# Optimization experiments

Hardware: AMD Instinct MI355X
Metric: run time of the kernel (lower is better)

Reference implementation:

```python
import jax, jax.numpy as jnp
import numpy as np

D_MODEL, N_HEADS, D_LLM = 1024, 16, 4096
D_KEYS = D_MODEL // N_HEADS  # 64


def setup_inputs() -> dict:
    key = jax.random.key(0)
    ks = jax.random.split(key, 11)
    s = lambda fan_in: 1.0 / np.sqrt(fan_in)
    inp = {
        "target_embedding": jax.random.normal(ks[0], (4, 2048, D_MODEL), jnp.float32),
        "source_embedding": jax.random.normal(ks[1], (4, 1024, D_LLM), jnp.float32),
        "value_embedding": jax.random.normal(ks[2], (4, 1024, D_LLM), jnp.float32),
        "Wq": jax.random.uniform(ks[3], (D_MODEL, D_KEYS * N_HEADS), jnp.float32, -s(D_MODEL), s(D_MODEL)),
        "bq": jax.random.uniform(ks[4], (D_KEYS * N_HEADS,), jnp.float32, -s(D_MODEL), s(D_MODEL)),
        "Wk": jax.random.uniform(ks[5], (D_LLM, D_KEYS * N_HEADS), jnp.float32, -s(D_LLM), s(D_LLM)),
        "bk": jax.random.uniform(ks[6], (D_KEYS * N_HEADS,), jnp.float32, -s(D_LLM), s(D_LLM)),
        "Wv": jax.random.uniform(ks[7], (D_LLM, D_KEYS * N_HEADS), jnp.float32, -s(D_LLM), s(D_LLM)),
        "bv": jax.random.uniform(ks[8], (D_KEYS * N_HEADS,), jnp.float32, -s(D_LLM), s(D_LLM)),
        "Wo": jax.random.uniform(ks[9], (D_KEYS * N_HEADS, D_MODEL), jnp.float32, -s(D_KEYS * N_HEADS), s(D_KEYS * N_HEADS)),
        "bo": jax.random.uniform(ks[10], (D_MODEL,), jnp.float32, -s(D_KEYS * N_HEADS), s(D_KEYS * N_HEADS)),
    }
    return inp


def reference(target_embedding, source_embedding, value_embedding,
              Wq, bq, Wk, bk, Wv, bv, Wo, bo):
    B, L, _ = target_embedding.shape
    _, S, _ = source_embedding.shape
    H, E = N_HEADS, D_KEYS
    q = (target_embedding @ Wq + bq).reshape(B, L, H, E)
    k = (source_embedding @ Wk + bk).reshape(B, S, H, E)
    v = (value_embedding @ Wv + bv).reshape(B, S, H, E)
    scale = 1.0 / np.sqrt(E)
    scores = jnp.einsum('blhe,bshe->bhls', q, k)  # [B,H,L,S]
    A = jax.nn.softmax(scale * scores, axis=-1)   # dropout = identity (eval mode)
    out = jnp.einsum('bhls,bshe->blhe', A, v).reshape(B, L, H * E)
    return out @ Wo + bo
```

## Files before the change

kernel.cpp:

```cpp
#include <hip/hip_runtime.h>
#include <hip/hip_bf16.h>

using bf16 = __hip_bfloat16;
typedef __attribute__((ext_vector_type(8))) short short8;
typedef __attribute__((ext_vector_type(4))) float f32x4;

static constexpr int Bc = 4, Lc = 2048, Sc = 1024;
static constexpr int DModel = 1024;

__device__ __forceinline__ void gload16(const void* g, void* l) {
  __builtin_amdgcn_global_load_lds((const __attribute__((address_space(1))) void*)g,
                                   (__attribute__((address_space(3))) void*)l,
                                   16, 0, 0);
}

__global__ void cvt3(const float* __restrict__ a, bf16* __restrict__ ao, long na4,
                     const float* __restrict__ b, bf16* __restrict__ bo, long nb4,
                     const float* __restrict__ c, bf16* __restrict__ co, long nc4) {
  long total = na4 + nb4 + nc4;
  long stride = (long)gridDim.x * blockDim.x;
  for (long i = (long)blockIdx.x * blockDim.x + threadIdx.x; i < total; i += stride) {
    const float* src; bf16* dst; long j;
    if (i < na4)            { src = a; dst = ao; j = i; }
    else if (i < na4 + nb4) { src = b; dst = bo; j = i - na4; }
    else                    { src = c; dst = co; j = i - na4 - nb4; }
    float4 v = reinterpret_cast<const float4*>(src)[j];
    alignas(8) bf16 t[4] = {__float2bfloat16(v.x), __float2bfloat16(v.y),
                            __float2bfloat16(v.z), __float2bfloat16(v.w)};
    reinterpret_cast<ushort4*>(dst)[j] = *reinterpret_cast<const ushort4*>(t);
  }
}

__global__ __launch_bounds__(256) void transpose_cvt_w(const float* __restrict__ Wq, bf16* __restrict__ WqT,
                                                       const float* __restrict__ Wk, bf16* __restrict__ WkT,
                                                       const float* __restrict__ Wv, bf16* __restrict__ WvT,
                                                       const float* __restrict__ Wo, bf16* __restrict__ WoT) {
  __shared__ bf16 tile[32][33];
  int bid = blockIdx.x;
  const float* in; bf16* out; int R, l;
  if (bid < 1024)      { in = Wq; out = WqT; R = 1024; l = bid; }
  else if (bid < 5120) { in = Wk; out = WkT; R = 4096; l = bid - 1024; }
  else if (bid < 9216) { in = Wv; out = WvT; R = 4096; l = bid - 5120; }
  else                 { in = Wo; out = WoT; R = 1024; l = bid - 9216; }
  const int C = 1024;
  int bx = l & 31, by = l >> 5;
  int tx = threadIdx.x & 31, ty = threadIdx.x >> 5;
  int r0 = by * 32, c0 = bx * 32;
#pragma unroll
  for (int i = 0; i < 32; i += 8)
    tile[ty + i][tx] = __float2bfloat16(in[(long)(r0 + ty + i) * C + c0 + tx]);
  __syncthreads();
#pragma unroll
  for (int i = 0; i < 32; i += 8)
    out[(long)(c0 + ty + i) * R + r0 + tx] = tile[tx][ty + i];
}

__device__ __forceinline__ void gemm_core(const bf16* __restrict__ A, const bf16* __restrict__ Bt,
                                          const float* __restrict__ bias,
                                          bf16* __restrict__ Cb, float* __restrict__ Cf,
                                          bf16* __restrict__ Cvt,
                                          int N, int K, int bx, int by,
                                          bf16* As, bf16* Bs) {
  const int tid = threadIdx.x;
  const int lane = tid & 63, g = lane >> 4, lm = lane & 15;
  const int wid = tid >> 6, wr = wid >> 1, wc = wid & 1;
  const long brow = (long)by * 128, bcol = (long)bx * 128;

  const bf16* asrc[4];
  const bf16* bsrc[4];
  int dsto[4];
#pragma unroll
  for (int t = 0; t < 4; ++t) {
    int sl = tid + t * 256;
    int row = sl >> 3;
    int kg = (sl & 7) ^ (row & 7);
    asrc[t] = A + (brow + row) * (long)K + kg * 8;
    bsrc[t] = Bt + (bcol + row) * (long)K + kg * 8;
    dsto[t] = sl * 16;
  }

  f32x4 zero = {0.f, 0.f, 0.f, 0.f};
  f32x4 acc[4][4];
#pragma unroll
  for (int i = 0; i < 4; ++i)
#pragma unroll
    for (int j = 0; j < 4; ++j) acc[i][j] = zero;

  char* Asc = (char*)As;
  char* Bsc = (char*)Bs;

#pragma unroll
  for (int t = 0; t < 4; ++t) {
    gload16(asrc[t], Asc + dsto[t]);
    gload16(bsrc[t], Bsc + dsto[t]);
    asrc[t] += 64; bsrc[t] += 64;
  }
  __syncthreads();

  const int nt = K >> 6;
  for (int i = 0; i < nt; ++i) {
    const int cur = i & 1;
    if (i + 1 < nt) {
      const int nxt = cur ^ 1;
#pragma unroll
      for (int t = 0; t < 4; ++t) {
        gload16(asrc[t], Asc + nxt * 16384 + dsto[t]);
        gload16(bsrc[t], Bsc + nxt * 16384 + dsto[t]);
        asrc[t] += 64; bsrc[t] += 64;
      }
    }
    const char* Ab = Asc + cur * 16384;
    const char* Bb = Bsc + cur * 16384;
    __builtin_amdgcn_s_setprio(1);
#pragma unroll
    for (int ks = 0; ks < 2; ++ks) {
      short8 af[4], bfv[4];
#pragma unroll
      for (int mi = 0; mi < 4; ++mi) {
        int m = wr * 64 + mi * 16 + lm;
        af[mi] = *reinterpret_cast<const short8*>(
            Ab + ((m * 128 + ks * 64 + g * 16) ^ ((m & 7) << 4)));
      }
#pragma unroll
      for (int ni = 0; ni < 4; ++ni) {
        int n = wc * 64 + ni * 16 + lm;
        bfv[ni] = *reinterpret_cast<const short8*>(
            Bb + ((n * 128 + ks * 64 + g * 16) ^ ((n & 7) << 4)));
      }
#pragma unroll
      for (int mi = 0; mi < 4; ++mi)
#pragma unroll
        for (int ni = 0; ni < 4; ++ni)
          acc[mi][ni] = __builtin_amdgcn_mfma_f32_16x16x32_bf16(af[mi], bfv[ni], acc[mi][ni], 0, 0, 0);
    }
    __builtin_amdgcn_s_setprio(0);
    __syncthreads();
  }

#pragma unroll
  for (int ni = 0; ni < 4; ++ni) {
    long n = bcol + wc * 64 + ni * 16 + lm;
    float bv = bias ? bias[n] : 0.f;
#pragma unroll
    for (int mi = 0; mi < 4; ++mi) {
      long m0 = brow + wr * 64 + mi * 16 + g * 4;
      if (Cvt) {
        long b = m0 >> 10, s0 = m0 & 1023;
        alignas(8) bf16 t4[4];
#pragma unroll
        for (int r = 0; r < 4; ++r) t4[r] = __float2bfloat16(acc[mi][ni][r] + bv);
        *reinterpret_cast<ushort4*>(Cvt + ((b << 10) + n) * 1024 + s0) =
            *reinterpret_cast<const ushort4*>(t4);
      } else {
#pragma unroll
        for (int r = 0; r < 4; ++r) {
          float o = acc[mi][ni][r] + bv;
          if (Cb) Cb[(m0 + r) * N + n] = __float2bfloat16(o);
          else    Cf[(m0 + r) * N + n] = o;
        }
      }
    }
  }
}

__global__ __launch_bounds__(256) void gemm_bt(const bf16* __restrict__ A,
                                               const bf16* __restrict__ Bt,
                                               const float* __restrict__ bias,
                                               bf16* __restrict__ Cb,
                                               float* __restrict__ Cf,
                                               int N, int K) {
  __shared__ bf16 As[2 * 128 * 64];
  __shared__ bf16 Bs[2 * 128 * 64];
  gemm_core(A, Bt, bias, Cb, Cf, nullptr, N, K, blockIdx.x, blockIdx.y, As, Bs);
}

__global__ __launch_bounds__(256) void gemm_qkv(
    const bf16* __restrict__ Ak, const bf16* __restrict__ Bk, const float* __restrict__ bk_, bf16* __restrict__ Ck, int Kk, int nbk,
    const bf16* __restrict__ Av, const bf16* __restrict__ Bv_, const float* __restrict__ bv_, bf16* __restrict__ CvT, int Kv, int nbv,
    const bf16* __restrict__ Aq, const bf16* __restrict__ Bq_, const float* __restrict__ bq_, bf16* __restrict__ Cq, int Kq) {
  __shared__ bf16 As[2 * 128 * 64];
  __shared__ bf16 Bs[2 * 128 * 64];
  int bid = blockIdx.x;
  const bf16 *A, *Bt; const float* bias; bf16 *C = nullptr, *Cvt = nullptr; int K, l;
  if (bid < nbk)            { A = Ak; Bt = Bk;  bias = bk_; C = Ck;    K = Kk; l = bid; }
  else if (bid < nbk + nbv) { A = Av; Bt = Bv_; bias = bv_; Cvt = CvT; K = Kv; l = bid - nbk; }
  else                      { A = Aq; Bt = Bq_; bias = bq_; C = Cq;   K = Kq; l = bid - nbk - nbv; }
  gemm_core(A, Bt, bias, C, nullptr, Cvt, 1024, K, l & 7, l >> 3, As, Bs);
}

__global__ __launch_bounds__(256) void attn_fused(const bf16* __restrict__ q,
                                                  const bf16* __restrict__ k,
                                                  const bf16* __restrict__ vT,
                                                  bf16* __restrict__ o) {
  constexpr float C2 = 0.18033688011112042f;
  constexpr float THR = 6.0f;
  __shared__ bf16 Kl[2][64 * 64];
  __shared__ bf16 Vl[2][64 * 64];
  __shared__ bf16 Pl[4][16 * 64];
  const int tid = threadIdx.x;
  const int lane = tid & 63, g = lane >> 4, lm = lane & 15;
  const int wid = tid >> 6;
  const int b = blockIdx.y >> 4, h = blockIdx.y & 15;
  const int qbase = blockIdx.x * 64 + wid * 16;

  const bf16* qrow = q + (long)(b * Lc + qbase + lm) * DModel + h * 64;
  short8 qa0 = *reinterpret_cast<const short8*>(qrow + g * 8);
  short8 qa1 = *reinterpret_cast<const short8*>(qrow + 32 + g * 8);
#pragma unroll
  for (int j = 0; j < 8; ++j) {
    union { ushort u; bf16 h; } cv;
    cv.u = (ushort)qa0[j];
    bf16 s0 = __float2bfloat16(__bfloat162float(cv.h) * C2);
    qa0[j] = (short)*reinterpret_cast<ushort*>(&s0);
    cv.u = (ushort)qa1[j];
    bf16 s1 = __float2bfloat16(__bfloat162float(cv.h) * C2);
    qa1[j] = (short)*reinterpret_cast<ushort*>(&s1);
  }

  const bf16* kbase = k + (long)b * Sc * DModel + h * 64;
  const bf16* vbase = vT + ((long)b * DModel + h * 64) * Sc;

  const bf16* ksrc[2];
  const bf16* vsrc[2];
  int dsto[2];
#pragma unroll
  for (int t = 0; t < 2; ++t) {
    int sl = tid + t * 256;
    int row = sl >> 3;
    int cg = (sl & 7) ^ (row & 7);
    ksrc[t] = kbase + (long)row * DModel + cg * 8;
    vsrc[t] = vbase + (long)row * Sc + cg * 8;
    dsto[t] = sl * 16;
  }

  f32x4 zero = {0.f, 0.f, 0.f, 0.f};
  f32x4 accO[4];
#pragma unroll
  for (int i = 0; i < 4; ++i) accO[i] = zero;
  f32x4 accL = zero;
  float mst[4] = {-1e30f, -1e30f, -1e30f, -1e30f};

  short8 vones;
#pragma unroll
  for (int j = 0; j < 8; ++j) vones[j] = (short)0x3F80;

  char* Klc = (char*)Kl;
  char* Vlc = (char*)Vl;
  char* Plc = (char*)Pl + wid * (16 * 64 * 2);

#pragma unroll
  for (int t = 0; t < 2; ++t) {
    gload16(ksrc[t], Klc + dsto[t]);
    gload16(vsrc[t], Vlc + dsto[t]);
    ksrc[t] += 64 * DModel; vsrc[t] += 64;
  }
  __syncthreads();

  for (int j = 0; j < Sc / 64; ++j) {
    const int cur = j & 1;
    if (j + 1 < Sc / 64) {
      const int nxt = cur ^ 1;
#pragma unroll
      for (int t = 0; t < 2; ++t) {
        gload16(ksrc[t], Klc + nxt * 8192 + dsto[t]);
        gload16(vsrc[t], Vlc + nxt * 8192 + dsto[t]);
        ksrc[t] += 64 * DModel; vsrc[t] += 64;
      }
    }
    const char* Kb = Klc + cur * 8192;
    const char* Vb = Vlc + cur * 8192;

    f32x4 scv[4];
    __builtin_amdgcn_s_setprio(1);
#pragma unroll
    for (int st = 0; st < 4; ++st) {
      int s = st * 16 + lm;
      int sw = (s & 7) << 4;
      short8 kb0 = *reinterpret_cast<const short8*>(Kb + ((s * 128 + g * 16) ^ sw));
      short8 kb1 = *reinterpret_cast<const short8*>(Kb + ((s * 128 + 64 + g * 16) ^ sw));
      f32x4 z = zero;
      z = __builtin_amdgcn_mfma_f32_16x16x32_bf16(qa0, kb0, z, 0, 0, 0);
      z = __builtin_amdgcn_mfma_f32_16x16x32_bf16(qa1, kb1, z, 0, 0, 0);
      scv[st] = z;
    }
    __builtin_amdgcn_s_setprio(0);

    float pmax[4];
#pragma unroll
    for (int r = 0; r < 4; ++r)
      pmax[r] = fmaxf(fmaxf(scv[0][r], scv[1][r]), fmaxf(scv[2][r], scv[3][r]));
    int need = 0;
#pragma unroll
    for (int r = 0; r < 4; ++r) need |= (pmax[r] > mst[r] + THR) ? 1 : 0;
    if (__any(need)) {
#pragma unroll
      for (int r = 0; r < 4; ++r) {
        float mx = pmax[r];
        mx = fmaxf(mx, __shfl_xor(mx, 1));
        mx = fmaxf(mx, __shfl_xor(mx, 2));
        mx = fmaxf(mx, __shfl_xor(mx, 4));
        mx = fmaxf(mx, __shfl_xor(mx, 8));
        float mnew = fmaxf(mst[r], mx);
        float corr = __builtin_amdgcn_exp2f(mst[r] - mnew);
        mst[r] = mnew;
        accL[r] *= corr;
#pragma unroll
        for (int et = 0; et < 4; ++et) accO[et][r] *= corr;
      }
    }
#pragma unroll
    for (int r = 0; r < 4; ++r) {
      int qq = g * 4 + r;
      int swp = (qq & 7) << 4;
#pragma unroll
      for (int st = 0; st < 4; ++st) {
        float p = __builtin_amdgcn_exp2f(scv[st][r] - mst[r]);
        *reinterpret_cast<bf16*>(Plc + ((qq * 128 + (st * 16 + lm) * 2) ^ swp)) =
            __float2bfloat16(p);
      }
    }

    __builtin_amdgcn_s_setprio(1);
#pragma unroll
    for (int sk = 0; sk < 2; ++sk) {
      short8 pa = *reinterpret_cast<const short8*>(
          Plc + ((lm * 128 + sk * 64 + g * 16) ^ ((lm & 7) << 4)));
      accL = __builtin_amdgcn_mfma_f32_16x16x32_bf16(pa, vones, accL, 0, 0, 0);
#pragma unroll
      for (int et = 0; et < 4; ++et) {
        int e = et * 16 + lm;
        short8 vb = *reinterpret_cast<const short8*>(
            Vb + ((e * 128 + sk * 64 + g * 16) ^ ((e & 7) << 4)));
        accO[et] = __builtin_amdgcn_mfma_f32_16x16x32_bf16(pa, vb, accO[et], 0, 0, 0);
      }
    }
    __builtin_amdgcn_s_setprio(0);
    __syncthreads();
  }

#pragma unroll
  for (int r = 0; r < 4; ++r) {
    float inv = 1.0f / accL[r];
    long row = (long)(b * Lc + qbase + g * 4 + r);
#pragma unroll
    for (int et = 0; et < 4; ++et)
      o[row * DModel + h * 64 + et * 16 + lm] = __float2bfloat16(accO[et][r] * inv);
  }
}

extern "C" void kernel_launch(void* const* d_in, const int* in_sizes, int n_in,
                              void* d_out, int out_size, void* d_ws, size_t ws_size,
                              hipStream_t stream) {
  const float* tgt = (const float*)d_in[0];
  const float* src = (const float*)d_in[1];
  const float* val = (const float*)d_in[2];
  const float* Wq  = (const float*)d_in[3];
  const float* bq  = (const float*)d_in[4];
  const float* Wk  = (const float*)d_in[5];
  const float* bk  = (const float*)d_in[6];
  const float* Wv  = (const float*)d_in[7];
  const float* bv  = (const float*)d_in[8];
  const float* Wo  = (const float*)d_in[9];
  const float* bo  = (const float*)d_in[10];
  float* out = (float*)d_out;
  char* ws = (char*)d_ws;

  const long n4_tgt = (long)8192 * 1024 / 4;
  const long n4_sv  = (long)4096 * 4096 / 4;

  if (ws_size < (132ul << 20)) return;

  bf16* WqT  = (bf16*)(ws + (0l   << 20));
  bf16* WkT  = (bf16*)(ws + (2l   << 20));
  bf16* WvT  = (bf16*)(ws + (10l  << 20));
  bf16* WoT  = (bf16*)(ws + (18l  << 20));
  bf16* tgtb = (bf16*)(ws + (20l  << 20));
  bf16* srcb = (bf16*)(ws + (36l  << 20));
  bf16* valb = (bf16*)(ws + (68l  << 20));
  bf16* qb   = (bf16*)(ws + (100l << 20));
  bf16* kb   = (bf16*)(ws + (116l << 20));
  bf16* vTb  = (bf16*)(ws + (124l << 20));
  bf16* attnb = tgtb;

  transpose_cvt_w<<<10240, 256, 0, stream>>>(Wq, WqT, Wk, WkT, Wv, WvT, Wo, WoT);
  cvt3<<<4096, 256, 0, stream>>>(tgt, tgtb, n4_tgt, src, srcb, n4_sv, val, valb, n4_sv);
  gemm_qkv<<<1024, 256, 0, stream>>>(srcb, WkT, bk, kb, 4096, 256,
                                     valb, WvT, bv, vTb, 4096, 256,
                                     tgtb, WqT, bq, qb, 1024);
  attn_fused<<<dim3(32, 64), 256, 0, stream>>>(qb, kb, vTb, attnb);
  gemm_bt<<<dim3(8, 64), 256, 0, stream>>>(attnb, WoT, bo, (bf16*)nullptr, out, 1024, 1024);
}
```

Before: 268.6 us.

## Use partial vmcnt waits with raw barriers and XCD-aware block remapping

Swaps __syncthreads for explicit s_waitcnt vmcnt(N) plus s_barrier in the GEMM and attention loops. Each tile then waits only for the loads of the current buffer while the prefetch of the next one stays in flight. It also flattens the attention and output-GEMM grids to 1D and remaps block IDs with an 8-way stride, so consecutive tiles that share operands land on the same XCD and its L2. The risk is that the hand-counted vmcnt values must match the number of outstanding global-to-LDS loads, or LDS reads could race.

```diff
diff --git a/kernel.cpp b/kernel.cpp
--- a/kernel.cpp
+++ b/kernel.cpp
@@ -13,6 +13,11 @@
                                    (__attribute__((address_space(3))) void*)l,
                                    16, 0, 0);
 }
+
+__device__ __forceinline__ void wait_vm8()  { asm volatile("s_waitcnt vmcnt(8)" ::: "memory"); }
+__device__ __forceinline__ void wait_vm4()  { asm volatile("s_waitcnt vmcnt(4)" ::: "memory"); }
+__device__ __forceinline__ void wait_vm0()  { asm volatile("s_waitcnt vmcnt(0)" ::: "memory"); }
+__device__ __forceinline__ void barrier_raw() { asm volatile("s_barrier" ::: "memory"); }
 
 __global__ void cvt3(const float* __restrict__ a, bf16* __restrict__ ao, long na4,
                      const float* __restrict__ b, bf16* __restrict__ bo, long nb4,
@@ -95,7 +100,6 @@
     gload16(bsrc[t], Bsc + dsto[t]);
     asrc[t] += 64; bsrc[t] += 64;
   }
-  __syncthreads();
 
   const int nt = K >> 6;
   for (int i = 0; i < nt; ++i) {
@@ -108,7 +112,12 @@
         gload16(bsrc[t], Bsc + nxt * 16384 + dsto[t]);
         asrc[t] += 64; bsrc[t] += 64;
       }
-    }
+      wait_vm8();
+    } else {
+      wait_vm0();
+    }
+    barrier_raw();
+
     const char* Ab = Asc + cur * 16384;
     const char* Bb = Bsc + cur * 16384;
     __builtin_amdgcn_s_setprio(1);
@@ -134,7 +143,7 @@
           acc[mi][ni] = __builtin_amdgcn_mfma_f32_16x16x32_bf16(af[mi], bfv[ni], acc[mi][ni], 0, 0, 0);
     }
     __builtin_amdgcn_s_setprio(0);
-    __syncthreads();
+    barrier_raw();
   }
 
 #pragma unroll
@@ -171,7 +180,9 @@
                                                int N, int K) {
   __shared__ bf16 As[2 * 128 * 64];
   __shared__ bf16 Bs[2 * 128 * 64];
-  gemm_core(A, Bt, bias, Cb, Cf, nullptr, N, K, blockIdx.x, blockIdx.y, As, Bs);
+  int bid = blockIdx.x;
+  int g = (bid & 7) * (gridDim.x >> 3) + (bid >> 3);
+  gemm_core(A, Bt, bias, Cb, Cf, nullptr, N, K, g & 7, g >> 3, As, Bs);
 }
 
 __global__ __launch_bounds__(256) void gemm_qkv(
@@ -181,11 +192,12 @@
   __shared__ bf16 As[2 * 128 * 64];
   __shared__ bf16 Bs[2 * 128 * 64];
   int bid = blockIdx.x;
-  const bf16 *A, *Bt; const float* bias; bf16 *C = nullptr, *Cvt = nullptr; int K, l;
-  if (bid < nbk)            { A = Ak; Bt = Bk;  bias = bk_; C = Ck;    K = Kk; l = bid; }
-  else if (bid < nbk + nbv) { A = Av; Bt = Bv_; bias = bv_; Cvt = CvT; K = Kv; l = bid - nbk; }
-  else                      { A = Aq; Bt = Bq_; bias = bq_; C = Cq;   K = Kq; l = bid - nbk - nbv; }
-  gemm_core(A, Bt, bias, C, nullptr, Cvt, 1024, K, l & 7, l >> 3, As, Bs);
+  const bf16 *A, *Bt; const float* bias; bf16 *C = nullptr, *Cvt = nullptr; int K, l, nb;
+  if (bid < nbk)            { A = Ak; Bt = Bk;  bias = bk_; C = Ck;    K = Kk; l = bid;             nb = nbk; }
+  else if (bid < nbk + nbv) { A = Av; Bt = Bv_; bias = bv_; Cvt = CvT; K = Kv; l = bid - nbk;       nb = nbv; }
+  else                      { A = Aq; Bt = Bq_; bias = bq_; C = Cq;   K = Kq; l = bid - nbk - nbv; nb = gridDim.x - nbk - nbv; }
+  int g = (l & 7) * (nb >> 3) + (l >> 3);
+  gemm_core(A, Bt, bias, C, nullptr, Cvt, 1024, K, g & 7, g >> 3, As, Bs);
 }
 
 __global__ __launch_bounds__(256) void attn_fused(const bf16* __restrict__ q,
@@ -200,8 +212,11 @@
   const int tid = threadIdx.x;
   const int lane = tid & 63, g = lane >> 4, lm = lane & 15;
   const int wid = tid >> 6;
-  const int b = blockIdx.y >> 4, h = blockIdx.y & 15;
-  const int qbase = blockIdx.x * 64 + wid * 16;
+  int bid = blockIdx.x;
+  int gl = (bid & 7) * 256 + (bid >> 3);
+  const int qt = gl & 31, bh = gl >> 5;
+  const int b = bh >> 4, h = bh & 15;
+  const int qbase = qt * 64 + wid * 16;
 
   const bf16* qrow = q + (long)(b * Lc + qbase + lm) * DModel + h * 64;
   short8 qa0 = *reinterpret_cast<const short8*>(qrow + g * 8);
@@ -254,7 +269,6 @@
     gload16(vsrc[t], Vlc + dsto[t]);
     ksrc[t] += 64 * DModel; vsrc[t] += 64;
   }
-  __syncthreads();
 
   for (int j = 0; j < Sc / 64; ++j) {
     const int cur = j & 1;
@@ -266,7 +280,12 @@
         gload16(vsrc[t], Vlc + nxt * 8192 + dsto[t]);
         ksrc[t] += 64 * DModel; vsrc[t] += 64;
       }
-    }
+      wait_vm4();
+    } else {
+      wait_vm0();
+    }
+    barrier_raw();
+
     const char* Kb = Klc + cur * 8192;
     const char* Vb = Vlc + cur * 8192;
 
@@ -335,7 +354,7 @@
       }
     }
     __builtin_amdgcn_s_setprio(0);
-    __syncthreads();
+    barrier_raw();
   }
 
 #pragma unroll
@@ -387,6 +406,6 @@
   gemm_qkv<<<1024, 256, 0, stream>>>(srcb, WkT, bk, kb, 4096, 256,
                                      valb, WvT, bv, vTb, 4096, 256,
                                      tgtb, WqT, bq, qb, 1024);
-  attn_fused<<<dim3(32, 64), 256, 0, stream>>>(qb, kb, vTb, attnb);
-  gemm_bt<<<dim3(8, 64), 256, 0, stream>>>(attnb, WoT, bo, (bf16*)nullptr, out, 1024, 1024);
-}
+  attn_fused<<<2048, 256, 0, stream>>>(qb, kb, vTb, attnb);
+  gemm_bt<<<512, 256, 0, stream>>>(attnb, WoT, bo, (bf16*)nullptr, out, 1024, 1024);
+}
```

Result: faster. 252.5 us (-6.0%).
